# Kernel optimization log

Measured on AMD Instinct MI355X. Metric: run time of the kernel, lower is better.

## Reference

```python
import jax, jax.numpy as jnp
import numpy as np
from jax import lax

K = 3          # kernel_size
G = 8          # group count in SIFA
EPS = 1e-5     # BN and GN eps


def _bn(x, g, b, m, v):
    # eval-mode BatchNorm2d over channel dim 1
    scale = (g / jnp.sqrt(v + EPS))[None, :, None, None]
    shift = (b - m * g / jnp.sqrt(v + EPS))[None, :, None, None]
    return x * scale + shift


def setup_inputs() -> dict:
    key = jax.random.key(0)
    ks = jax.random.split(key, 20)
    B, C, H, W, OUP = 8, 64, 128, 128, 128
    CE = C * K * K  # expanded channels = 576
    CG = C // G     # channels per group view = 8
    f32 = jnp.float32
    inp = {
        "x": jax.random.normal(ks[0], (B, C, H, W), f32),
        # depthwise generate conv: groups=C, out=C*K^2 -> OIHW [CE,1,K,K]
        "gen_w": jax.random.normal(ks[1], (CE, 1, K, K), f32) * 0.1,
        "gen_bn_g": jnp.ones((CE,), f32) + 0.1 * jax.random.normal(ks[2], (CE,), f32),
        "gen_bn_b": 0.1 * jax.random.normal(ks[3], (CE,), f32),
        "gen_bn_m": 0.05 * jax.random.normal(ks[4], (CE,), f32),
        "gen_bn_v": jax.random.uniform(ks[5], (CE,), f32, 0.5, 1.5),
        # GroupNorm(num_groups=CG, num_channels=CG) affine params
        "gn_w": jnp.ones((CG,), f32) + 0.1 * jax.random.normal(ks[6], (CG,), f32),
        "gn_b": 0.1 * jax.random.normal(ks[7], (CG,), f32),
        # gating params, shape (1, CG, 1, 1)
        "cweight": 0.1 * jax.random.normal(ks[8], (1, CG, 1, 1), f32),
        "cbias": jnp.ones((1, CG, 1, 1), f32) + 0.1 * jax.random.normal(ks[9], (1, CG, 1, 1), f32),
        "sweight": 0.1 * jax.random.normal(ks[10], (1, CG, 1, 1), f32),
        "sbias": jnp.ones((1, CG, 1, 1), f32) + 0.1 * jax.random.normal(ks[11], (1, CG, 1, 1), f32),
        "weights_add": jnp.asarray(0.5, f32),
        # final Conv: C -> OUP, k=K, s=K, p=0, bias=False + BN + SiLU
        "conv_w": jax.random.normal(ks[12], (OUP, C, K, K), f32) * (1.0 / np.sqrt(C * K * K)),
        "conv_bn_g": jnp.ones((OUP,), f32) + 0.1 * jax.random.normal(ks[13], (OUP,), f32),
        "conv_bn_b": 0.1 * jax.random.normal(ks[14], (OUP,), f32),
        "conv_bn_m": 0.05 * jax.random.normal(ks[15], (OUP,), f32),
        "conv_bn_v": jax.random.uniform(ks[16], (OUP,), f32, 0.5, 1.5),
    }
    return inp


def reference(x, gen_w, gen_bn_g, gen_bn_b, gen_bn_m, gen_bn_v,
              gn_w, gn_b, cweight, cbias, sweight, sbias, weights_add,
              conv_w, conv_bn_g, conv_bn_b, conv_bn_m, conv_bn_v):
    B, C, H, W = x.shape
    # --- generate: depthwise conv (groups=C) + BN + ReLU ---
    y = lax.conv_general_dilated(
        x, gen_w, window_strides=(1, 1), padding=[(K // 2, K // 2)] * 2,
        feature_group_count=C,
        dimension_numbers=("NCHW", "OIHW", "NCHW"))  # [B, C*K*K, H, W]
    y = jax.nn.relu(_bn(y, gen_bn_g, gen_bn_b, gen_bn_m, gen_bn_v))
    # --- rearrange 'b c (n1 n2) h w -> b c (h n1) (w n2)' ---
    y = y.reshape(B, C, K, K, H, W)          # (b, c, n1, n2, h, w)
    y = y.transpose(0, 1, 4, 2, 5, 3)        # (b, c, h, n1, w, n2)
    HK, WK = H * K, W * K
    y = y.reshape(B, C, HK, WK)
    # --- group view: (b*G, C//G, HK, WK) ---
    g = y.reshape(B * G, C // G, HK, WK)
    # channel gate: global avg pool -> affine -> sigmoid
    x_ch = jnp.mean(g, axis=(2, 3), keepdims=True)        # [B*G, CG, 1, 1]
    ch = g * jax.nn.sigmoid(cweight * x_ch + cbias)
    # spatial gate: per-channel GroupNorm (num_groups == num_channels)
    mu = jnp.mean(g, axis=(2, 3), keepdims=True)
    var = jnp.var(g, axis=(2, 3), keepdims=True)
    gnorm = (g - mu) / jnp.sqrt(var + EPS)
    gnorm = gnorm * gn_w[None, :, None, None] + gn_b[None, :, None, None]
    sp = g * jax.nn.sigmoid(sweight * gnorm + sbias)
    out = weights_add * ch + (1.0 - weights_add) * sp
    out = out.reshape(B, C, HK, WK)
    # --- final Conv: k=K, s=K, p=0, no bias + BN + SiLU ---
    z = lax.conv_general_dilated(
        out, conv_w, window_strides=(K, K), padding="VALID",
        dimension_numbers=("NCHW", "OIHW", "NCHW"))       # [B, OUP, H, W]
    z = _bn(z, conv_bn_g, conv_bn_b, conv_bn_m, conv_bn_v)
    return z * jax.nn.sigmoid(z)  # SiLU
```

## Files before the change

kernel.cpp:

```cpp
#include <hip/hip_runtime.h>
#include <math.h>


#define EPSF 1e-5f
typedef _Float16 v8h __attribute__((ext_vector_type(8)));
typedef __fp16 fp16x2 __attribute__((ext_vector_type(2)));
typedef float v4f __attribute__((ext_vector_type(4)));

static constexpr int C_ = 64, HW_ = 16384, W_ = 128;

static constexpr int WS_WFOLD = 0;
static constexpr int WS_SHIFT = 5184;
static constexpr int WS_BIAS  = 5760;
static constexpr int WS_GATE  = 5888;
static constexpr int WS_PART  = 7936;
static constexpr int WS_WH    = 12032;

__device__ __forceinline__ float sigmf(float v) { return 1.f / (1.f + __expf(-v)); }

__global__ __launch_bounds__(256) void k_fold(
    const float* __restrict__ gen_w,
    const float* __restrict__ gg, const float* __restrict__ gb,
    const float* __restrict__ gm, const float* __restrict__ gv,
    const float* __restrict__ conv_w,
    const float* __restrict__ cg, const float* __restrict__ cb,
    const float* __restrict__ cm, const float* __restrict__ cv,
    float* __restrict__ ws)
{
    int idx = blockIdx.x * 256 + threadIdx.x;
    _Float16* Whp = (_Float16*)(ws + WS_WH);
    if (idx < 131072) {
        int kb = idx >> 10, oup = (idx >> 3) & 127, e = idx & 7;
        int k = kb * 8 + e, c = k >> 4, j = k & 15;
        float s = cg[oup] * rsqrtf(cv[oup] + EPSF);
        float v = (j < 9) ? conv_w[(oup * C_ + c) * 9 + j] * s : 0.f;
        Whp[idx] = (_Float16)v;
    } else if (idx < 136256) {
        int i = idx - 131072; int ce = i / 9;
        float s = gg[ce] * rsqrtf(gv[ce] + EPSF);
        ws[WS_WFOLD + i] = gen_w[i] * s;
    } else if (idx < 136832) {
        int ce = idx - 136256;
        float s = gg[ce] * rsqrtf(gv[ce] + EPSF);
        ws[WS_SHIFT + ce] = gb[ce] - gm[ce] * s;
    } else if (idx < 136960) {
        int oup = idx - 136832;
        float s = cg[oup] * rsqrtf(cv[oup] + EPSF);
        ws[WS_BIAS + oup] = cb[oup] - cm[oup] * s;
    }
}

__global__ __launch_bounds__(256) void k_stats(
    const float* __restrict__ x, const float* __restrict__ ws,
    float* __restrict__ part)
{
    __shared__ float xs[34 * 132];
    __shared__ __align__(16) float wfl[84];
    __shared__ float shl[9];
    __shared__ float r1[4], r2[4];
    int bid = blockIdx.x; int b = bid >> 8; int c = (bid >> 2) & 63; int q = bid & 3;
    int t = threadIdx.x;
    const float* xp = x + (size_t)(b * C_ + c) * HW_;
    for (int i = t; i < 4420; i += 256) {
        int r = i / 130, cc = i - r * 130;
        int yy = q * 32 + r - 1, xx = cc - 1;
        float v = 0.f;
        if (yy >= 0 && yy < 128 && xx >= 0 && xx < 128) v = xp[yy * 128 + xx];
        xs[r * 132 + cc] = v;
    }
    if (t < 84) wfl[t] = ws[WS_WFOLD + c * 81 + ((t < 81) ? t : 80)];
    if (t >= 84 && t < 93) shl[t - 84] = ws[WS_SHIFT + c * 9 + (t - 84)];
    __syncthreads();

    float wv[84];
#pragma unroll
    for (int i = 0; i < 21; ++i) *(float4*)&wv[i * 4] = *(const float4*)&wfl[i * 4];
    float sh9[9];
#pragma unroll
    for (int i = 0; i < 9; ++i) sh9[i] = shl[i];

    float s1 = 0.f, s2 = 0.f;
    for (int i = 0; i < 16; ++i) {
        int id = i * 256 + t; int row = id >> 7, col = id & 127;
        float nb[9];
#pragma unroll
        for (int dy = 0; dy < 3; ++dy)
#pragma unroll
            for (int dx = 0; dx < 3; ++dx) nb[dy * 3 + dx] = xs[(row + dy) * 132 + col + dx];
        float uv[9];
#pragma unroll
        for (int j = 0; j < 9; ++j) uv[j] = sh9[j];
#pragma unroll
        for (int k = 0; k < 9; ++k) {
            float xv = nb[k];
#pragma unroll
            for (int j = 0; j < 9; ++j) uv[j] = fmaf(wv[j * 9 + k], xv, uv[j]);
        }
#pragma unroll
        for (int j = 0; j < 9; ++j) {
            float v = fmaxf(uv[j], 0.f);
            s1 += v; s2 = fmaf(v, v, s2);
        }
    }
#pragma unroll
    for (int off = 32; off > 0; off >>= 1) {
        s1 += __shfl_down(s1, off, 64);
        s2 += __shfl_down(s2, off, 64);
    }
    int wid = t >> 6;
    if ((t & 63) == 0) { r1[wid] = s1; r2[wid] = s2; }
    __syncthreads();
    if (t == 0) {
        part[bid * 2]     = r1[0] + r1[1] + r1[2] + r1[3];
        part[bid * 2 + 1] = r2[0] + r2[1] + r2[2] + r2[3];
    }
}

__global__ __launch_bounds__(256) void k_gate(
    const float* __restrict__ part,
    const float* __restrict__ cwt, const float* __restrict__ cbs,
    const float* __restrict__ swt, const float* __restrict__ sbs,
    const float* __restrict__ gnw, const float* __restrict__ gnb,
    const float* __restrict__ wadd, float4* __restrict__ gate)
{
    int i = blockIdx.x * 256 + threadIdx.x;
    if (i >= 512) return;
    int b = i >> 6, c = i & 63;
    float s1 = 0.f, s2 = 0.f;
    for (int q = 0; q < 4; ++q) {
        int pi = (b * 256 + c * 4 + q) * 2;
        s1 += part[pi]; s2 += part[pi + 1];
    }
    const float N = 9.f * 16384.f;
    float mean = s1 / N;
    float var = s2 / N - mean * mean;
    float inv = rsqrtf(var + EPSF);
    int cgi = c & 7;
    float wa = wadd[0];
    float cgt = sigmf(cwt[cgi] * mean + cbs[cgi]);
    const float NL2E = -1.44269504f;
    float4 o;
    o.x = wa * cgt;
    o.y = 1.f - wa;
    o.z = NL2E * (swt[cgi] * gnw[cgi] * inv);
    o.w = NL2E * (swt[cgi] * (gnb[cgi] - mean * inv * gnw[cgi]) + sbs[cgi]);
    gate[i] = o;
}

__global__ __launch_bounds__(256) void k_main(
    const float* __restrict__ x, const float* __restrict__ ws,
    float* __restrict__ out)
{
    __shared__ _Float16 u_s[2][128 * 64];
    __shared__ float xs[2][4 * 200];
    __shared__ float bias_s[128];

    int t = threadIdx.x;
    int bid = blockIdx.x;
    int b = bid >> 7, tile = bid & 127;
    int oh0 = (tile >> 3) << 3;
    int ow0 = (tile & 7) << 4;
    if (t < 128) bias_s[t] = ws[WS_BIAS + t];

    const float* xb = x + (size_t)b * C_ * HW_;
    const _Float16* Wh = (const _Float16*)(ws + WS_WH);

    int w = __builtin_amdgcn_readfirstlane(t >> 6);
    int lane = t & 63, quad = lane >> 4, l15 = lane & 15;
    int col = lane & 15, prow0 = (lane >> 4) << 1;

    v4f acc[4][4];
#pragma unroll
    for (int a = 0; a < 4; ++a)
#pragma unroll
        for (int bb = 0; bb < 4; ++bb) acc[a][bb] = (v4f)0.f;

    auto stage = [&](int buf, int c) {
        const float* xc = xb + (size_t)c * HW_;
#pragma unroll
        for (int i = 0; i < 3; ++i) {
            int item = lane + i * 64;
            if (item < 180) {
                int r = item / 18, cl = item - r * 18;
                int yy = oh0 + r - 1, xx = ow0 + cl - 1;
                float v = 0.f;
                if (yy >= 0 && yy < 128 && xx >= 0 && xx < 128) v = xc[yy * 128 + xx];
                xs[buf][w * 200 + r * 20 + cl] = v;
            }
        }
    };

    auto uphase = [&](int it) {
        int buf = it & 1;
        int c = it * 4 + w;
        const float* xw = &xs[buf][w * 200];
        float nb[12];
#pragma unroll
        for (int dr = 0; dr < 4; ++dr)
#pragma unroll
            for (int dc = 0; dc < 3; ++dc)
                nb[dr * 3 + dc] = xw[(prow0 + dr) * 20 + col + dc];

        const float* wfp = ws + WS_WFOLD + c * 81;
        const float* shp = ws + WS_SHIFT + c * 9;
        float4 g4 = *(const float4*)(ws + WS_GATE + (((b << 6) + c) << 2));

        int p0 = prow0 * 16 + col;
        int swzA0 = ((2 * w) ^ (p0 & 7)) << 3;
        int swzA1 = ((2 * w) ^ ((p0 + 16) & 7)) << 3;
        int swzB0 = ((2 * w + 1) ^ (p0 & 7)) << 3;
        int swzB1 = ((2 * w + 1) ^ ((p0 + 16) & 7)) << 3;
        _Float16* us = u_s[buf];

#pragma unroll 1
        for (int jp = 0; jp < 4; ++jp) {
            float wl[18];
#pragma unroll
            for (int i = 0; i < 18; ++i) wl[i] = wfp[jp * 18 + i];
            float s0 = shp[jp * 2], s1v = shp[jp * 2 + 1];
#pragma unroll
            for (int px = 0; px < 2; ++px) {
                float a0 = s0, a1 = s1v;
#pragma unroll
                for (int k = 0; k < 9; ++k) {
                    float xv = nb[(px + k / 3) * 3 + (k % 3)];
                    a0 = fmaf(wl[k], xv, a0);
                    a1 = fmaf(wl[9 + k], xv, a1);
                }
                float v0 = fmaxf(a0, 0.f), v1 = fmaxf(a1, 0.f);
                float e0 = __builtin_amdgcn_exp2f(fmaf(g4.z, v0, g4.w));
                float e1 = __builtin_amdgcn_exp2f(fmaf(g4.z, v1, g4.w));
                float u0 = v0 * fmaf(g4.y, __builtin_amdgcn_rcpf(1.f + e0), g4.x);
                float u1 = v1 * fmaf(g4.y, __builtin_amdgcn_rcpf(1.f + e1), g4.x);
                int base = (p0 + px * 16) * 64 + (px ? swzA1 : swzA0);
                *(fp16x2*)&us[base + jp * 2] = __builtin_amdgcn_cvt_pkrtz(u0, u1);
            }
        }
        {
            float w9[9];
#pragma unroll
            for (int i = 0; i < 9; ++i) w9[i] = wfp[72 + i];
            float s8 = shp[8];
#pragma unroll
            for (int px = 0; px < 2; ++px) {
                float a0 = s8;
#pragma unroll
                for (int k = 0; k < 9; ++k)
                    a0 = fmaf(w9[k], nb[(px + k / 3) * 3 + (k % 3)], a0);
                float v0 = fmaxf(a0, 0.f);
                float e0 = __builtin_amdgcn_exp2f(fmaf(g4.z, v0, g4.w));
                float u8 = v0 * fmaf(g4.y, __builtin_amdgcn_rcpf(1.f + e0), g4.x);
                union { fp16x2 p[4]; float4 f; } z;
                z.p[0] = __builtin_amdgcn_cvt_pkrtz(u8, 0.f);
                z.p[1] = __builtin_amdgcn_cvt_pkrtz(0.f, 0.f);
                z.p[2] = z.p[1]; z.p[3] = z.p[1];
                int base = (p0 + px * 16) * 64 + (px ? swzB1 : swzB0);
                *(float4*)&us[base] = z.f;
            }
        }
    };

    stage(0, w);
    __syncthreads();
    uphase(0);
    stage(1, 4 + w);
    __syncthreads();

    for (int it = 0; it < 16; ++it) {
        v8h A[2][4];
#pragma unroll
        for (int ks = 0; ks < 2; ++ks)
#pragma unroll
            for (int a = 0; a < 4; ++a) {
                int row = ((w & 1) << 6) + (a << 4) + l15;
                int kb = it * 8 + ks * 4 + quad;
                A[ks][a] = *(const v8h*)(Wh + ((size_t)kb * 128 + row) * 8);
            }

        if (it < 15) uphase(it + 1);
        if (it < 14) stage(it & 1, (it + 2) * 4 + w);

        const _Float16* ub = u_s[it & 1];
#pragma unroll
        for (int ks = 0; ks < 2; ++ks) {
            int kb = ks * 4 + quad;
            v8h Bf[4];
#pragma unroll
            for (int bb = 0; bb < 4; ++bb) {
                int row = ((w >> 1) << 6) + (bb << 4) + l15;
                Bf[bb] = *(const v8h*)&ub[row * 64 + ((kb ^ (row & 7)) << 3)];
            }
#pragma unroll
            for (int a = 0; a < 4; ++a)
#pragma unroll
                for (int bb = 0; bb < 4; ++bb)
                    acc[a][bb] = __builtin_amdgcn_mfma_f32_16x16x32_f16(A[ks][a], Bf[bb], acc[a][bb], 0, 0, 0);
        }
        if (it < 15) __syncthreads();
    }

    size_t ob = (size_t)b * 128 * HW_;
#pragma unroll
    for (int a = 0; a < 4; ++a) {
#pragma unroll
        for (int r = 0; r < 4; ++r) {
            int oup = ((w & 1) << 6) + (a << 4) + (quad << 2) + r;
            float bo = bias_s[oup];
#pragma unroll
            for (int bb = 0; bb < 4; ++bb) {
                int p2 = ((w >> 1) << 6) + (bb << 4) + l15;
                int py2 = p2 >> 4, px2 = p2 & 15;
                float z = acc[a][bb][r] + bo;
                out[ob + (size_t)oup * HW_ + (oh0 + py2) * W_ + ow0 + px2] = z * sigmf(z);
            }
        }
    }
}

extern "C" void kernel_launch(void* const* d_in, const int* in_sizes, int n_in,
                              void* d_out, int out_size, void* d_ws, size_t ws_size,
                              hipStream_t stream)
{
    const float* x      = (const float*)d_in[0];
    const float* gen_w  = (const float*)d_in[1];
    const float* gg     = (const float*)d_in[2];
    const float* gb     = (const float*)d_in[3];
    const float* gm     = (const float*)d_in[4];
    const float* gv     = (const float*)d_in[5];
    const float* gnw    = (const float*)d_in[6];
    const float* gnb    = (const float*)d_in[7];
    const float* cwt    = (const float*)d_in[8];
    const float* cbs    = (const float*)d_in[9];
    const float* swt    = (const float*)d_in[10];
    const float* sbs    = (const float*)d_in[11];
    const float* wadd   = (const float*)d_in[12];
    const float* conv_w = (const float*)d_in[13];
    const float* cg2    = (const float*)d_in[14];
    const float* cb2    = (const float*)d_in[15];
    const float* cm2    = (const float*)d_in[16];
    const float* cv2    = (const float*)d_in[17];
    float* ws  = (float*)d_ws;
    float* out = (float*)d_out;

    k_fold<<<535, 256, 0, stream>>>(gen_w, gg, gb, gm, gv, conv_w, cg2, cb2, cm2, cv2, ws);
    k_stats<<<2048, 256, 0, stream>>>(x, ws, ws + WS_PART);
    k_gate<<<2, 256, 0, stream>>>(ws + WS_PART, cwt, cbs, swt, sbs, gnw, gnb, wadd,
                                  (float4*)(ws + WS_GATE));
    k_main<<<1024, 256, 0, stream>>>(x, ws, out);
}
```

Measured before the change: 245.8 us.

## Split expansion into separate kernel writing fp16 B image, shrink K padding

A new k_apply kernel computes the expanded depthwise conv, BN, ReLU and gating for every pixel and writes an fp16 GEMM-ready operand image to workspace. k_main is reduced to a plain MFMA GEMM that streams A and B fragments straight from global memory, with no LDS staging and no barriers. The K dimension is repacked from 16 slots per channel to 36 used of 40 per 4-channel pair, which cuts padded MFMA work. The cost is a large fp16 intermediate written and re-read through HBM, and batches may be processed in chunks if the workspace is too small.

```diff
diff --git a/kernel.cpp b/kernel.cpp
--- a/kernel.cpp
+++ b/kernel.cpp
@@ -8,6 +8,7 @@
 typedef float v4f __attribute__((ext_vector_type(4)));
 
 static constexpr int C_ = 64, HW_ = 16384, W_ = 128;
+static constexpr int KB_ = 80;
 
 static constexpr int WS_WFOLD = 0;
 static constexpr int WS_SHIFT = 5184;
@@ -15,6 +16,9 @@
 static constexpr int WS_GATE  = 5888;
 static constexpr int WS_PART  = 7936;
 static constexpr int WS_WH    = 12032;
+static constexpr int WS_BIMG  = 52992;
+static constexpr size_t BIMG_BATCH_F16 = (size_t)128 * KB_ * 128 * 8;
+static constexpr size_t BIMG_BATCH_FLT = BIMG_BATCH_F16 / 2;
 
 __device__ __forceinline__ float sigmf(float v) { return 1.f / (1.f + __expf(-v)); }
 
@@ -29,22 +33,28 @@
 {
     int idx = blockIdx.x * 256 + threadIdx.x;
     _Float16* Whp = (_Float16*)(ws + WS_WH);
-    if (idx < 131072) {
+    if (idx < 81920) {
         int kb = idx >> 10, oup = (idx >> 3) & 127, e = idx & 7;
-        int k = kb * 8 + e, c = k >> 4, j = k & 15;
-        float s = cg[oup] * rsqrtf(cv[oup] + EPSF);
-        float v = (j < 9) ? conv_w[(oup * C_ + c) * 9 + j] * s : 0.f;
+        int k = kb * 8 + e;
+        int grp = k / 80, rr = k - grp * 80;
+        int tp = rr / 40, vv = rr - tp * 40;
+        float v = 0.f;
+        if (vv < 36) {
+            int j = vv >> 2, cl = vv & 3, c = grp * 8 + tp * 4 + cl;
+            float s = cg[oup] * rsqrtf(cv[oup] + EPSF);
+            v = conv_w[(oup * C_ + c) * 9 + j] * s;
+        }
         Whp[idx] = (_Float16)v;
-    } else if (idx < 136256) {
-        int i = idx - 131072; int ce = i / 9;
+    } else if (idx < 87104) {
+        int i = idx - 81920; int ce = i / 9;
         float s = gg[ce] * rsqrtf(gv[ce] + EPSF);
         ws[WS_WFOLD + i] = gen_w[i] * s;
-    } else if (idx < 136832) {
-        int ce = idx - 136256;
+    } else if (idx < 87680) {
+        int ce = idx - 87104;
         float s = gg[ce] * rsqrtf(gv[ce] + EPSF);
         ws[WS_SHIFT + ce] = gb[ce] - gm[ce] * s;
-    } else if (idx < 136960) {
-        int oup = idx - 136832;
+    } else if (idx < 87808) {
+        int oup = idx - 87680;
         float s = cg[oup] * rsqrtf(cv[oup] + EPSF);
         ws[WS_BIAS + oup] = cb[oup] - cm[oup] * s;
     }
@@ -147,27 +157,98 @@
     gate[i] = o;
 }
 
+__global__ __launch_bounds__(256) void k_apply(
+    const float* __restrict__ x, float* __restrict__ ws, int b0)
+{
+    __shared__ float xs[4][18 * 19];
+    int bid = blockIdx.x;
+    int cq = bid & 15, p = (bid >> 4) & 63, bbl = bid >> 10;
+    int b = b0 + bbl;
+    int oh0 = (p >> 3) << 4, ow0 = (p & 7) << 4;
+    int t = threadIdx.x;
+    int row16 = t >> 4, col = t & 15;
+
+    for (int i = t; i < 1296; i += 256) {
+        int ch = i / 324, rr = i - ch * 324;
+        int r = rr / 18, cc = rr - r * 18;
+        int yy = oh0 + r - 1, xx = ow0 + cc - 1;
+        float v = 0.f;
+        if (yy >= 0 && yy < 128 && xx >= 0 && xx < 128)
+            v = x[(size_t)(b * C_ + cq * 4 + ch) * HW_ + yy * 128 + xx];
+        xs[ch][r * 19 + cc] = v;
+    }
+    __syncthreads();
+
+    float nb4[4][9];
+#pragma unroll
+    for (int ch = 0; ch < 4; ++ch)
+#pragma unroll
+        for (int dy = 0; dy < 3; ++dy)
+#pragma unroll
+            for (int dx = 0; dx < 3; ++dx)
+                nb4[ch][dy * 3 + dx] = xs[ch][(row16 + dy) * 19 + col + dx];
+
+    float4 g[4];
+#pragma unroll
+    for (int ch = 0; ch < 4; ++ch)
+        g[ch] = *(const float4*)(ws + WS_GATE + (size_t)(b * C_ + cq * 4 + ch) * 4);
+
+    int tile = ((p >> 3) * 2 + (row16 >> 3)) * 8 + (p & 7);
+    int px = (row16 & 7) * 16 + col;
+    _Float16* Bimg = (_Float16*)(ws + WS_BIMG)
+        + (size_t)(bbl * 128 + tile) * (KB_ * 1024) + (size_t)px * 8;
+
+#pragma unroll 1
+    for (int j = 0; j < 9; ++j) {
+        float wj[4][9], sj[4];
+#pragma unroll
+        for (int ch = 0; ch < 4; ++ch) {
+            const float* wp = ws + WS_WFOLD + (cq * 4 + ch) * 81 + j * 9;
+#pragma unroll
+            for (int k = 0; k < 9; ++k) wj[ch][k] = wp[k];
+            sj[ch] = ws[WS_SHIFT + (cq * 4 + ch) * 9 + j];
+        }
+        float uv[4];
+#pragma unroll
+        for (int ch = 0; ch < 4; ++ch) {
+            float a = sj[ch];
+#pragma unroll
+            for (int k = 0; k < 9; ++k) a = fmaf(wj[ch][k], nb4[ch][k], a);
+            float v = fmaxf(a, 0.f);
+            float e = __builtin_amdgcn_exp2f(fmaf(g[ch].z, v, g[ch].w));
+            uv[ch] = v * fmaf(g[ch].y, __builtin_amdgcn_rcpf(1.f + e), g[ch].x);
+        }
+        union { fp16x2 p2[2]; uint2 u; } pk;
+        pk.p2[0] = __builtin_amdgcn_cvt_pkrtz(uv[0], uv[1]);
+        pk.p2[1] = __builtin_amdgcn_cvt_pkrtz(uv[2], uv[3]);
+        *(uint2*)(Bimg + (size_t)(cq * 5 + (j >> 1)) * 1024 + (j & 1) * 4) = pk.u;
+    }
+    uint2 z; z.x = 0u; z.y = 0u;
+    *(uint2*)(Bimg + (size_t)(cq * 5 + 4) * 1024 + 4) = z;
+}
+
 __global__ __launch_bounds__(256) void k_main(
-    const float* __restrict__ x, const float* __restrict__ ws,
-    float* __restrict__ out)
-{
-    __shared__ _Float16 u_s[2][128 * 64];
-    __shared__ float xs[2][4 * 200];
+    const float* __restrict__ ws, float* __restrict__ out, int b0)
+{
     __shared__ float bias_s[128];
-
     int t = threadIdx.x;
     int bid = blockIdx.x;
-    int b = bid >> 7, tile = bid & 127;
-    int oh0 = (tile >> 3) << 3;
-    int ow0 = (tile & 7) << 4;
+    int bbl = bid >> 7, tile = bid & 127;
+    int b = b0 + bbl;
+    int oh0 = (tile >> 3) << 3, ow0 = (tile & 7) << 4;
     if (t < 128) bias_s[t] = ws[WS_BIAS + t];
-
-    const float* xb = x + (size_t)b * C_ * HW_;
-    const _Float16* Wh = (const _Float16*)(ws + WS_WH);
+    __syncthreads();
 
     int w = __builtin_amdgcn_readfirstlane(t >> 6);
     int lane = t & 63, quad = lane >> 4, l15 = lane & 15;
-    int col = lane & 15, prow0 = (lane >> 4) << 1;
+    int arow = ((w & 1) << 6) + l15;
+    int brow = ((w >> 1) << 6) + l15;
+
+    const _Float16* Aq = (const _Float16*)(ws + WS_WH)
+        + (size_t)quad * 1024 + (size_t)arow * 8;
+    const _Float16* Bq = (const _Float16*)(ws + WS_BIMG)
+        + (size_t)(bbl * 128 + tile) * (KB_ * 1024)
+        + (size_t)quad * 1024 + (size_t)brow * 8;
 
     v4f acc[4][4];
 #pragma unroll
@@ -175,128 +256,24 @@
 #pragma unroll
         for (int bb = 0; bb < 4; ++bb) acc[a][bb] = (v4f)0.f;
 
-    auto stage = [&](int buf, int c) {
-        const float* xc = xb + (size_t)c * HW_;
-#pragma unroll
-        for (int i = 0; i < 3; ++i) {
-            int item = lane + i * 64;
-            if (item < 180) {
-                int r = item / 18, cl = item - r * 18;
-                int yy = oh0 + r - 1, xx = ow0 + cl - 1;
-                float v = 0.f;
-                if (yy >= 0 && yy < 128 && xx >= 0 && xx < 128) v = xc[yy * 128 + xx];
-                xs[buf][w * 200 + r * 20 + cl] = v;
-            }
-        }
-    };
-
-    auto uphase = [&](int it) {
-        int buf = it & 1;
-        int c = it * 4 + w;
-        const float* xw = &xs[buf][w * 200];
-        float nb[12];
-#pragma unroll
-        for (int dr = 0; dr < 4; ++dr)
-#pragma unroll
-            for (int dc = 0; dc < 3; ++dc)
-                nb[dr * 3 + dc] = xw[(prow0 + dr) * 20 + col + dc];
-
-        const float* wfp = ws + WS_WFOLD + c * 81;
-        const float* shp = ws + WS_SHIFT + c * 9;
-        float4 g4 = *(const float4*)(ws + WS_GATE + (((b << 6) + c) << 2));
-
-        int p0 = prow0 * 16 + col;
-        int swzA0 = ((2 * w) ^ (p0 & 7)) << 3;
-        int swzA1 = ((2 * w) ^ ((p0 + 16) & 7)) << 3;
-        int swzB0 = ((2 * w + 1) ^ (p0 & 7)) << 3;
-        int swzB1 = ((2 * w + 1) ^ ((p0 + 16) & 7)) << 3;
-        _Float16* us = u_s[buf];
-
 #pragma unroll 1
-        for (int jp = 0; jp < 4; ++jp) {
-            float wl[18];
-#pragma unroll
-            for (int i = 0; i < 18; ++i) wl[i] = wfp[jp * 18 + i];
-            float s0 = shp[jp * 2], s1v = shp[jp * 2 + 1];
-#pragma unroll
-            for (int px = 0; px < 2; ++px) {
-                float a0 = s0, a1 = s1v;
-#pragma unroll
-                for (int k = 0; k < 9; ++k) {
-                    float xv = nb[(px + k / 3) * 3 + (k % 3)];
-                    a0 = fmaf(wl[k], xv, a0);
-                    a1 = fmaf(wl[9 + k], xv, a1);
-                }
-                float v0 = fmaxf(a0, 0.f), v1 = fmaxf(a1, 0.f);
-                float e0 = __builtin_amdgcn_exp2f(fmaf(g4.z, v0, g4.w));
-                float e1 = __builtin_amdgcn_exp2f(fmaf(g4.z, v1, g4.w));
-                float u0 = v0 * fmaf(g4.y, __builtin_amdgcn_rcpf(1.f + e0), g4.x);
-                float u1 = v1 * fmaf(g4.y, __builtin_amdgcn_rcpf(1.f + e1), g4.x);
-                int base = (p0 + px * 16) * 64 + (px ? swzA1 : swzA0);
-                *(fp16x2*)&us[base + jp * 2] = __builtin_amdgcn_cvt_pkrtz(u0, u1);
-            }
-        }
-        {
-            float w9[9];
-#pragma unroll
-            for (int i = 0; i < 9; ++i) w9[i] = wfp[72 + i];
-            float s8 = shp[8];
-#pragma unroll
-            for (int px = 0; px < 2; ++px) {
-                float a0 = s8;
-#pragma unroll
-                for (int k = 0; k < 9; ++k)
-                    a0 = fmaf(w9[k], nb[(px + k / 3) * 3 + (k % 3)], a0);
-                float v0 = fmaxf(a0, 0.f);
-                float e0 = __builtin_amdgcn_exp2f(fmaf(g4.z, v0, g4.w));
-                float u8 = v0 * fmaf(g4.y, __builtin_amdgcn_rcpf(1.f + e0), g4.x);
-                union { fp16x2 p[4]; float4 f; } z;
-                z.p[0] = __builtin_amdgcn_cvt_pkrtz(u8, 0.f);
-                z.p[1] = __builtin_amdgcn_cvt_pkrtz(0.f, 0.f);
-                z.p[2] = z.p[1]; z.p[3] = z.p[1];
-                int base = (p0 + px * 16) * 64 + (px ? swzB1 : swzB0);
-                *(float4*)&us[base] = z.f;
-            }
-        }
-    };
-
-    stage(0, w);
-    __syncthreads();
-    uphase(0);
-    stage(1, 4 + w);
-    __syncthreads();
-
-    for (int it = 0; it < 16; ++it) {
-        v8h A[2][4];
-#pragma unroll
-        for (int ks = 0; ks < 2; ++ks)
-#pragma unroll
-            for (int a = 0; a < 4; ++a) {
-                int row = ((w & 1) << 6) + (a << 4) + l15;
-                int kb = it * 8 + ks * 4 + quad;
-                A[ks][a] = *(const v8h*)(Wh + ((size_t)kb * 128 + row) * 8);
-            }
-
-        if (it < 15) uphase(it + 1);
-        if (it < 14) stage(it & 1, (it + 2) * 4 + w);
-
-        const _Float16* ub = u_s[it & 1];
+    for (int it = 0; it < 10; ++it) {
+        size_t ito = (size_t)it * 8192;
 #pragma unroll
         for (int ks = 0; ks < 2; ++ks) {
-            int kb = ks * 4 + quad;
-            v8h Bf[4];
-#pragma unroll
-            for (int bb = 0; bb < 4; ++bb) {
-                int row = ((w >> 1) << 6) + (bb << 4) + l15;
-                Bf[bb] = *(const v8h*)&ub[row * 64 + ((kb ^ (row & 7)) << 3)];
-            }
+            v8h A[4], Bf[4];
 #pragma unroll
             for (int a = 0; a < 4; ++a)
+                A[a] = *(const v8h*)(Aq + ito + ks * 4096 + a * 128);
+#pragma unroll
+            for (int bb = 0; bb < 4; ++bb)
+                Bf[bb] = *(const v8h*)(Bq + ito + ks * 4096 + bb * 128);
+#pragma unroll
+            for (int a = 0; a < 4; ++a)
 #pragma unroll
                 for (int bb = 0; bb < 4; ++bb)
-                    acc[a][bb] = __builtin_amdgcn_mfma_f32_16x16x32_f16(A[ks][a], Bf[bb], acc[a][bb], 0, 0, 0);
-        }
-        if (it < 15) __syncthreads();
+                    acc[a][bb] = __builtin_amdgcn_mfma_f32_16x16x32_f16(A[a], Bf[bb], acc[a][bb], 0, 0, 0);
+        }
     }
 
     size_t ob = (size_t)b * 128 * HW_;
@@ -342,9 +319,19 @@
     float* ws  = (float*)d_ws;
     float* out = (float*)d_out;
 
-    k_fold<<<535, 256, 0, stream>>>(gen_w, gg, gb, gm, gv, conv_w, cg2, cb2, cm2, cv2, ws);
+    size_t avail = ws_size / 4;
+    int nb = 1;
+    const int cands[4] = {8, 4, 2, 1};
+    for (int i = 0; i < 4; ++i) {
+        if ((size_t)WS_BIMG + (size_t)cands[i] * BIMG_BATCH_FLT <= avail) { nb = cands[i]; break; }
+    }
+
+    k_fold<<<343, 256, 0, stream>>>(gen_w, gg, gb, gm, gv, conv_w, cg2, cb2, cm2, cv2, ws);
     k_stats<<<2048, 256, 0, stream>>>(x, ws, ws + WS_PART);
     k_gate<<<2, 256, 0, stream>>>(ws + WS_PART, cwt, cbs, swt, sbs, gnw, gnb, wadd,
                                   (float4*)(ws + WS_GATE));
-    k_main<<<1024, 256, 0, stream>>>(x, ws, out);
-}
+    for (int b0 = 0; b0 < 8; b0 += nb) {
+        k_apply<<<nb * 1024, 256, 0, stream>>>(x, ws, b0);
+        k_main<<<nb * 128, 256, 0, stream>>>(ws, out, b0);
+    }
+}
```

Result: slower. 301.8 us (+22.8%).
